# Performance work log

Measured on AMD Instinct MI355X. Metric: run time of the kernel, lower is better.

The kernel has to match this reference:

```python
import jax, jax.numpy as jnp
import numpy as np
from jax import lax

D_MODEL, D_STATE, D_CONV, EXPAND, HEADDIM = 1024, 128, 4, 2, 64
D_INNER = EXPAND * D_MODEL            # 2048
NHEADS = D_INNER // HEADDIM           # 32
CONV_DIM = D_INNER + 2 * D_STATE      # 2304 (ngroups=1)
D_IN_PROJ = 2 * D_INNER + 2 * D_STATE + NHEADS  # 4384


def setup_inputs() -> dict:
    key = jax.random.key(0)
    ks = jax.random.split(key, 9)
    b, l = 2, 2048
    x = jax.random.normal(ks[0], (b, l, D_MODEL), jnp.float32)
    in_proj_w = jax.random.normal(ks[1], (D_IN_PROJ, D_MODEL), jnp.float32) * 0.02
    conv_w = jax.random.normal(ks[2], (CONV_DIM, D_CONV), jnp.float32) * 0.2
    conv_b = jax.random.normal(ks[3], (CONV_DIM,), jnp.float32) * 0.02
    dt_bias = jnp.log(jnp.expm1(jax.random.uniform(ks[4], (NHEADS,), jnp.float32, 0.001, 0.1)))
    A_log = jnp.log(jax.random.uniform(ks[5], (NHEADS,), jnp.float32, 1.0, 16.0))
    D = jax.random.normal(ks[6], (NHEADS,), jnp.float32)
    norm_w = jnp.ones((D_INNER,), jnp.float32)
    out_proj_w = jax.random.normal(ks[7], (D_MODEL, D_INNER), jnp.float32) * 0.02
    return {"x": x, "in_proj_w": in_proj_w, "conv_w": conv_w, "conv_b": conv_b,
            "dt_bias": dt_bias, "A_log": A_log, "D": D, "norm_w": norm_w,
            "out_proj_w": out_proj_w}


def _mamba2(x, in_proj_w, conv_w, conv_b, dt_bias, A_log, D, norm_w, out_proj_w):
    b, l, _ = x.shape
    zxbcdt = x @ in_proj_w.T  # (b,l,D_IN_PROJ)
    z = zxbcdt[..., :D_INNER]
    xBC = zxbcdt[..., D_INNER:D_INNER + CONV_DIM]
    dt = zxbcdt[..., D_INNER + CONV_DIM:]  # (b,l,h)
    # causal depthwise conv1d + SiLU
    xBC_pad = jnp.pad(xBC, ((0, 0), (D_CONV - 1, 0), (0, 0)))
    windows = jnp.stack([xBC_pad[:, k:k + l, :] for k in range(D_CONV)], axis=-1)  # (b,l,c,K)
    xBC = jax.nn.silu(jnp.einsum('blck,ck->blc', windows, conv_w) + conv_b)
    xs = xBC[..., :D_INNER]
    B = xBC[..., D_INNER:D_INNER + D_STATE]   # (b,l,n)
    C = xBC[..., D_INNER + D_STATE:]          # (b,l,n)
    xh = xs.reshape(b, l, NHEADS, HEADDIM)
    dt = jax.nn.softplus(dt + dt_bias)        # (b,l,h)
    A = -jnp.exp(A_log)                       # (h,)
    dA = jnp.exp(dt * A)                      # (b,l,h)
    xdt = xh * dt[..., None]                  # (b,l,h,p)

    def step(S, inp):
        dA_t, xdt_t, B_t, C_t = inp  # (b,h),(b,h,p),(b,n),(b,n)
        S = dA_t[:, :, None, None] * S + xdt_t[..., None] * B_t[:, None, None, :]
        y_t = jnp.einsum('bhpn,bn->bhp', S, C_t)
        return S, y_t

    S0 = jnp.zeros((b, NHEADS, HEADDIM, D_STATE), x.dtype)
    _, y = lax.scan(step, S0,
                    (dA.transpose(1, 0, 2), xdt.transpose(1, 0, 2, 3),
                     B.transpose(1, 0, 2), C.transpose(1, 0, 2)))
    y = y.transpose(1, 0, 2, 3) + D[None, None, :, None] * xh  # (b,l,h,p)
    y = y.reshape(b, l, D_INNER)
    # gated RMSNorm: norm(y * silu(z)) * weight
    y = y * jax.nn.silu(z)
    y = y * lax.rsqrt(jnp.mean(y * y, axis=-1, keepdims=True) + 1e-5) * norm_w
    return y @ out_proj_w.T


def reference(x, in_proj_w, conv_w, conv_b, dt_bias, A_log, D, norm_w, out_proj_w):
    return x + _mamba2(x, in_proj_w, conv_w, conv_b, dt_bias, A_log, D, norm_w, out_proj_w)
```

## Files before the change

### kernel.cpp

```cpp
#include <hip/hip_runtime.h>
#include <hip/hip_bf16.h>
#include <cstdint>

typedef __hip_bfloat16 bf16;
typedef __attribute__((ext_vector_type(8))) short short8;
typedef __attribute__((ext_vector_type(4))) float f32x4;
typedef unsigned int u32;

#define BB 2
#define LL 2048
#define DM 1024
#define DI 2048
#define DS 128
#define NH 32
#define HD 64
#define CONVD 2304
#define DPROJ 4384
#define DPAD 4480
#define NBL (BB*LL)
#define NCHK 16
#define CLEN 128

__device__ __forceinline__ float bf2f(bf16 v) { return __bfloat162float(v); }
__device__ __forceinline__ bf16 f2bf(float f) { return __float2bfloat16(f); }
__device__ __forceinline__ unsigned short f2bfu(float f) {
  bf16 t = __float2bfloat16(f); return *(unsigned short*)&t;
}
__device__ __forceinline__ float bfu2f(unsigned short u) {
  u32 b = ((u32)u) << 16; return *(float*)&b;
}

__device__ __forceinline__ void gload16(const void* g, void* l) {
  __builtin_amdgcn_global_load_lds(
      (const __attribute__((address_space(1))) u32*)g,
      (__attribute__((address_space(3))) u32*)l, 16, 0, 0);
}

template<int N> __device__ __forceinline__ void waitvm() {
  __builtin_amdgcn_sched_barrier(0);
  if constexpr (N == 0) asm volatile("s_waitcnt vmcnt(0)" ::: "memory");
  else if constexpr (N == 3) asm volatile("s_waitcnt vmcnt(3)" ::: "memory");
  else if constexpr (N == 4) asm volatile("s_waitcnt vmcnt(4)" ::: "memory");
  __builtin_amdgcn_sched_barrier(0);
}
__device__ __forceinline__ void rawbar() {
  __builtin_amdgcn_sched_barrier(0);
  __builtin_amdgcn_s_barrier();
  __builtin_amdgcn_sched_barrier(0);
}

__global__ __launch_bounds__(256)
void k_cast3(const float* __restrict__ s0, bf16* __restrict__ d0, int n0,
             const float* __restrict__ s1, bf16* __restrict__ d1, int n1,
             const float* __restrict__ s2, bf16* __restrict__ d2, int n2)
{
  int i = blockIdx.x * blockDim.x + threadIdx.x;
  const int stride = gridDim.x * blockDim.x;
  const int total = n0 + n1 + n2;
  for (; i < total; i += stride) {
    const float* s; bf16* d; int j = i;
    if (j < n0)            { s = s0; d = d0; }
    else if (j < n0 + n1)  { s = s1; d = d1; j -= n0; }
    else                   { s = s2; d = d2; j -= n0 + n1; }
    const float4 v = ((const float4*)s)[j];
    u32 w0 = (u32)f2bfu(v.x) | ((u32)f2bfu(v.y) << 16);
    u32 w1 = (u32)f2bfu(v.z) | ((u32)f2bfu(v.w) << 16);
    *(uint2*)(d + (size_t)j*4) = make_uint2(w0, w1);
  }
}

template<int TM, int MODE>
__global__ __launch_bounds__(512)
void k_gemm_nt(const bf16* __restrict__ A, const bf16* __restrict__ W,
               int K, int Nw, int ldo,
               float* __restrict__ outf, const bf16* __restrict__ residb,
               bf16* __restrict__ outb, float* __restrict__ dtraw)
{
  constexpr int BUFE = (TM + 128) * 64;
  constexpr int LPT  = TM/64 + 2;
  __shared__ __align__(16) unsigned short S[2*BUFE];
  const int tid = threadIdx.x;
  const int w = tid >> 6, lane = tid & 63;
  const int m0 = blockIdx.x * TM, n0 = blockIdx.y * 128;
  const int wr = w >> 2, wc = w & 3;
  constexpr int MI = TM / 32;
  f32x4 acc[MI][2] = {};
  const int r0 = lane & 15;
  const int kq = (lane >> 4) * 8;
  const int srow = lane >> 3;
  const int scol = ((lane & 7) ^ (lane >> 3)) << 3;
  const int swz  = (r0 & 7) << 3;
  const int NT = K >> 6;

#define STAGE(T, BUF) {                                                          \
    const int k0s = (T) << 6;                                                    \
    unsigned short* dst = S + (BUF) * BUFE;                                      \
    _Pragma("unroll")                                                            \
    for (int it = 0; it < TM/64; ++it) {                                         \
      const int seg = it*8 + w;                                                  \
      const int row = seg*8 + srow;                                              \
      gload16(A + (size_t)(m0 + row)*K + (k0s + scol), (char*)dst + seg*1024);   \
    }                                                                            \
    unsigned short* dstW = dst + TM*64;                                          \
    _Pragma("unroll")                                                            \
    for (int it = 0; it < 2; ++it) {                                             \
      const int seg = it*8 + w;                                                  \
      const int row = seg*8 + srow;                                              \
      int rw = n0 + row; rw = (rw < Nw) ? rw : (Nw - 1);                         \
      gload16(W + (size_t)rw*K + (k0s + scol), (char*)dstW + seg*1024);          \
    }                                                                            \
  }

  STAGE(0, 0);
  STAGE(1, 1);
  waitvm<LPT>();
  rawbar();

  for (int t = 0; t < NT; ++t) {
    const int cur = t & 1;
    const unsigned short* As = S + cur*BUFE;
    const unsigned short* Ws = As + TM*64;
    #pragma unroll
    for (int kk = 0; kk < 64; kk += 32) {
      const int ce = (kk + kq) ^ swz;
      short8 af[MI], bw[2];
      #pragma unroll
      for (int mi = 0; mi < MI; ++mi)
        af[mi] = *(const short8*)(As + (wr*(TM/2) + mi*16 + r0)*64 + ce);
      #pragma unroll
      for (int ni = 0; ni < 2; ++ni)
        bw[ni] = *(const short8*)(Ws + (wc*32 + ni*16 + r0)*64 + ce);
      #pragma unroll
      for (int mi = 0; mi < MI; ++mi)
        #pragma unroll
        for (int ni = 0; ni < 2; ++ni)
          acc[mi][ni] = __builtin_amdgcn_mfma_f32_16x16x32_bf16(af[mi], bw[ni], acc[mi][ni], 0, 0, 0);
    }
    rawbar();
    if (t + 2 < NT) {
      STAGE(t + 2, cur);
      waitvm<LPT>();
      rawbar();
    } else if (t + 1 < NT) {
      waitvm<0>();
      rawbar();
    }
  }
#undef STAGE

  const int rr = (lane >> 4) * 4;
  if (MODE == 0) {
    #pragma unroll
    for (int mi = 0; mi < MI; ++mi) {
      #pragma unroll
      for (int ni = 0; ni < 2; ++ni) {
        const int col = n0 + wc*32 + ni*16 + r0;
        #pragma unroll
        for (int r = 0; r < 4; ++r) {
          const int row = m0 + wr*(TM/2) + mi*16 + rr + r;
          outf[(size_t)row*ldo + col] =
              acc[mi][ni][r] + bf2f(residb[(size_t)row*ldo + col]);
        }
      }
    }
  } else {
    if (n0 == 4352 && wc == 0) {
      #pragma unroll
      for (int ni = 0; ni < 2; ++ni)
        #pragma unroll
        for (int mi = 0; mi < MI; ++mi)
          #pragma unroll
          for (int r = 0; r < 4; ++r) {
            const int row = m0 + wr*(TM/2) + mi*16 + rr + r;
            dtraw[(size_t)row*NH + ni*16 + r0] = acc[mi][ni][r];
          }
    }
    #pragma unroll
    for (int mi = 0; mi < MI; ++mi) {
      #pragma unroll
      for (int ni = 0; ni < 2; ++ni) {
        const int colt = wc*32 + ni*16 + r0;
        #pragma unroll
        for (int r = 0; r < 4; ++r) {
          const int rowt = wr*(TM/2) + mi*16 + rr + r;
          const int g = (colt >> 3) ^ (rowt & 7);
          S[rowt*128 + g*8 + (colt & 7)] = f2bfu(acc[mi][ni][r]);
        }
      }
    }
    __syncthreads();
    const int row = tid >> 2, j4 = tid & 3;
    unsigned short* orow = (unsigned short*)outb + (size_t)(m0 + row)*ldo + n0 + j4*32;
    #pragma unroll
    for (int jj = 0; jj < 4; ++jj) {
      const int g = (j4*4 + jj) ^ (row & 7);
      *(short8*)(orow + jj*8) = *(const short8*)&S[row*128 + g*8];
    }
  }
}

__global__ __launch_bounds__(256)
void k_conv(const bf16* __restrict__ zxb, const float* __restrict__ dtraw,
            const float* __restrict__ convw, const float* __restrict__ convb,
            const float* __restrict__ dtb, const float* __restrict__ alog,
            bf16* __restrict__ xs, float* __restrict__ dt,
            float* __restrict__ ldA, bf16* __restrict__ Bc, bf16* __restrict__ Cc)
{
  const int bl = ((blockIdx.x & 7) << 9) | (blockIdx.x >> 3);
  const int l = bl & (LL - 1);
  const int tid = threadIdx.x;
  if (tid < NH) {
    float raw = dtraw[(size_t)bl*NH + tid] + dtb[tid];
    float sp = (raw > 20.f) ? raw : log1pf(__expf(raw));
    float Ah = -__expf(alog[tid]);
    dt[(size_t)bl*NH + tid] = sp;
    ldA[(size_t)bl*NH + tid] = sp * Ah;
  }
  for (int g = tid; g < CONVD/8; g += 256) {
    const int c0 = g*8;
    float acc[8];
    float4 wv[8];
    #pragma unroll
    for (int e = 0; e < 8; ++e) wv[e] = ((const float4*)convw)[c0 + e];
    {
      const float4 b0 = *(const float4*)(convb + c0);
      const float4 b1 = *(const float4*)(convb + c0 + 4);
      acc[0]=b0.x; acc[1]=b0.y; acc[2]=b0.z; acc[3]=b0.w;
      acc[4]=b1.x; acc[5]=b1.y; acc[6]=b1.z; acc[7]=b1.w;
    }
    #pragma unroll
    for (int k = 0; k < 4; ++k) {
      if (l - 3 + k >= 0) {
        short8 v = *(const short8*)((const unsigned short*)zxb + (size_t)(bl - 3 + k)*DPAD + DI + c0);
        #pragma unroll
        for (int e = 0; e < 8; ++e) {
          const float wk = (k == 0) ? wv[e].x : (k == 1) ? wv[e].y : (k == 2) ? wv[e].z : wv[e].w;
          acc[e] = fmaf(bfu2f((unsigned short)v[e]), wk, acc[e]);
        }
      }
    }
    short8 ov;
    #pragma unroll
    for (int e = 0; e < 8; ++e) {
      const float s = acc[e] / (1.f + __expf(-acc[e]));
      ov[e] = (short)f2bfu(s);
    }
    if (c0 < DI)            *(short8*)((unsigned short*)xs + (size_t)bl*DI + c0) = ov;
    else if (c0 < DI + DS)  *(short8*)((unsigned short*)Bc + (size_t)bl*DS + (c0 - DI)) = ov;
    else                    *(short8*)((unsigned short*)Cc + (size_t)bl*DS + (c0 - DI - DS)) = ov;
  }
}

__global__ __launch_bounds__(256)
void k_bt(const bf16* __restrict__ Bc, bf16* __restrict__ BT)
{
  const int bidx2 = blockIdx.x;
  const int b = bidx2 >> 4, c = bidx2 & 15;
  const int bl0 = b*LL + c*CLEN;
  __shared__ unsigned short LT[128*132];
  const int tid = threadIdx.x;
  {
    const int ts = tid >> 3, seg = tid & 7;
    #pragma unroll
    for (int r = 0; r < 4; ++r) {
      const int t = r*32 + ts;
      const unsigned short* src = (const unsigned short*)(Bc + (size_t)(bl0 + t)*DS);
      short8 v0 = *(const short8*)(src + seg*16);
      short8 v1 = *(const short8*)(src + seg*16 + 8);
      u32 w0 = (u32)(unsigned short)v0[0] | ((u32)(unsigned short)v0[1] << 16);
      u32 w1 = (u32)(unsigned short)v0[2] | ((u32)(unsigned short)v0[3] << 16);
      u32 w2 = (u32)(unsigned short)v0[4] | ((u32)(unsigned short)v0[5] << 16);
      u32 w3 = (u32)(unsigned short)v0[6] | ((u32)(unsigned short)v0[7] << 16);
      u32 w4 = (u32)(unsigned short)v1[0] | ((u32)(unsigned short)v1[1] << 16);
      u32 w5 = (u32)(unsigned short)v1[2] | ((u32)(unsigned short)v1[3] << 16);
      u32 w6 = (u32)(unsigned short)v1[4] | ((u32)(unsigned short)v1[5] << 16);
      u32 w7 = (u32)(unsigned short)v1[6] | ((u32)(unsigned short)v1[7] << 16);
      uint2* d = (uint2*)&LT[t*132 + seg*16];
      d[0] = make_uint2(w0, w1); d[1] = make_uint2(w2, w3);
      d[2] = make_uint2(w4, w5); d[3] = make_uint2(w6, w7);
    }
  }
  __syncthreads();
  {
    const int n = tid >> 1, th = tid & 1;
    unsigned short* dst = (unsigned short*)(BT + (size_t)bidx2*16384 + n*128 + th*64);
    #pragma unroll
    for (int j = 0; j < 8; ++j) {
      short8 o;
      #pragma unroll
      for (int e = 0; e < 8; ++e)
        o[e] = (short)LT[(th*64 + j*8 + e)*132 + n];
      *(short8*)(dst + j*8) = o;
    }
  }
}

__global__ __launch_bounds__(512)
void k_xt_state(const bf16* __restrict__ xs, const float* __restrict__ dt,
                const bf16* __restrict__ BT, const float* __restrict__ ldA,
                bf16* __restrict__ xT, unsigned short* __restrict__ Sloc,
                float* __restrict__ clog)
{
  const int bidx = blockIdx.x;
  const int c = bidx & 15, h = (bidx >> 4) & 31, b = bidx >> 9;
  const int bl0 = b*LL + c*CLEN;
  const int bidx2 = b*NCHK + c;
  __shared__ unsigned short LT[128*68];
  __shared__ __align__(16) unsigned short XWs[64*136];
  __shared__ float w1[128];
  const int tid = threadIdx.x;
  const int w = tid >> 6, lane = tid & 63;
  const int r0 = lane & 15, kq = (lane >> 4) * 8;
  short8 bfr[4];
  #pragma unroll
  for (int kk = 0; kk < 4; ++kk)
    bfr[kk] = *(const short8*)((const unsigned short*)BT + (size_t)bidx2*16384
                               + (size_t)(w*16 + r0)*128 + kk*32 + kq);
  {
    const int ts = tid >> 3, seg = tid & 7;
    #pragma unroll
    for (int r = 0; r < 2; ++r) {
      const int t = r*64 + ts;
      const float dtv = dt[(size_t)(bl0 + t)*NH + h];
      short8 v = *(const short8*)((const unsigned short*)(xs + (size_t)(bl0 + t)*DI + h*HD) + seg*8);
      unsigned short o[8];
      #pragma unroll
      for (int e = 0; e < 8; ++e)
        o[e] = f2bfu(bfu2f((unsigned short)v[e]) * dtv);
      uint2* d = (uint2*)&LT[t*68 + seg*8];
      d[0] = make_uint2((u32)o[0] | ((u32)o[1] << 16), (u32)o[2] | ((u32)o[3] << 16));
      d[1] = make_uint2((u32)o[4] | ((u32)o[5] << 16), (u32)o[6] | ((u32)o[7] << 16));
    }
  }
  if (tid < 64) {
    const int ln = tid;
    const float a0 = ldA[(size_t)(bl0 + 2*ln)*NH + h];
    const float a1 = ldA[(size_t)(bl0 + 2*ln + 1)*NH + h];
    float s = a0 + a1;
    #pragma unroll
    for (int off = 1; off < 64; off <<= 1) {
      const float v = __shfl_up(s, off);
      if (ln >= off) s += v;
    }
    const float Ltot = __shfl(s, 63);
    w1[2*ln + 1] = __expf(Ltot - s);
    w1[2*ln]     = __expf(Ltot - (s - a1));
    if (ln == 63) clog[bidx] = Ltot;
  }
  __syncthreads();
  {
    const int p = tid >> 3, tg = tid & 7;
    unsigned short* xdst = (unsigned short*)xT + (size_t)bidx*8192 + p*128 + tg*16;
    #pragma unroll
    for (int half = 0; half < 2; ++half) {
      short8 oXT, oXW;
      #pragma unroll
      for (int e = 0; e < 8; ++e) {
        const int t = tg*16 + half*8 + e;
        const unsigned short u = LT[t*68 + p];
        oXT[e] = (short)u;
        oXW[e] = (short)f2bfu(bfu2f(u) * w1[t]);
      }
      *(short8*)(xdst + half*8) = oXT;
      *(short8*)&XWs[p*136 + tg*16 + half*8] = oXW;
    }
  }
  __syncthreads();
  f32x4 acc[4] = {};
  #pragma unroll
  for (int kk = 0; kk < 4; ++kk) {
    #pragma unroll
    for (int mi = 0; mi < 4; ++mi) {
      short8 a = *(const short8*)&XWs[(mi*16 + r0)*136 + kk*32 + kq];
      acc[mi] = __builtin_amdgcn_mfma_f32_16x16x32_bf16(a, bfr[kk], acc[mi], 0, 0, 0);
    }
  }
  const int rr = (lane >> 4) * 4;
  unsigned short* So = Sloc + (size_t)bidx*8192;
  #pragma unroll
  for (int mi = 0; mi < 4; ++mi)
    #pragma unroll
    for (int r = 0; r < 4; ++r)
      So[(mi*16 + rr + r)*128 + w*16 + r0] = f2bfu(acc[mi][r]);
}

__global__ __launch_bounds__(256)
void k_chunk_combine(unsigned short* __restrict__ Sloc, const float* __restrict__ clog)
{
  const int bh = blockIdx.x >> 3;
  const int e0 = ((blockIdx.x & 7) * 256 + threadIdx.x) * 4;
  float t0 = 0.f, t1 = 0.f, t2 = 0.f, t3 = 0.f;
  for (int c = 0; c < NCHK; ++c) {
    unsigned short* Sp = Sloc + ((size_t)(bh*NCHK + c))*8192 + e0;
    const uint2 raw = *(const uint2*)Sp;
    const float l0 = bfu2f((unsigned short)(raw.x & 0xffff));
    const float l1 = bfu2f((unsigned short)(raw.x >> 16));
    const float l2 = bfu2f((unsigned short)(raw.y & 0xffff));
    const float l3 = bfu2f((unsigned short)(raw.y >> 16));
    uint2 o;
    o.x = (u32)f2bfu(t0) | ((u32)f2bfu(t1) << 16);
    o.y = (u32)f2bfu(t2) | ((u32)f2bfu(t3) << 16);
    *(uint2*)Sp = o;
    const float P = __expf(clog[bh*NCHK + c]);
    t0 = P*t0 + l0; t1 = P*t1 + l1; t2 = P*t2 + l2; t3 = P*t3 + l3;
  }
}

__global__ __launch_bounds__(512)
void k_scan(const bf16* __restrict__ xT, const bf16* __restrict__ Bc,
            const bf16* __restrict__ Cc, const unsigned short* __restrict__ Sinit,
            const float* __restrict__ ldA, const bf16* __restrict__ xs,
            const float* __restrict__ Dv, unsigned short* __restrict__ y)
{
  const int bidx = blockIdx.x;
  const int c = bidx & 15, h = (bidx >> 4) & 31, b = bidx >> 9;
  const int bl0 = b*LL + c*CLEN;
  __shared__ __align__(16) unsigned short Bs[128*136];
  __shared__ __align__(16) unsigned short XDs[64*136];
  __shared__ __align__(16) unsigned short SIs[64*136];
  __shared__ float la[128];
  const int tid = threadIdx.x;
  const int w = tid >> 6, lane = tid & 63;
  const int r0 = lane & 15, kq = (lane >> 4) * 8;
  short8 cfr[4];
  #pragma unroll
  for (int kk = 0; kk < 4; ++kk)
    cfr[kk] = *(const short8*)((const unsigned short*)Cc
                               + (size_t)(bl0 + w*16 + r0)*DS + kk*32 + kq);
  {
    const int t = tid >> 2, sg = tid & 3;
    const unsigned short* sb = (const unsigned short*)(Bc + (size_t)(bl0 + t)*DS) + sg*32;
    #pragma unroll
    for (int j = 0; j < 4; ++j)
      *(short8*)&Bs[t*136 + sg*32 + j*8] = *(const short8*)(sb + j*8);
  }
  {
    const int p = tid >> 3, seg = tid & 7;
    const unsigned short* sx = (const unsigned short*)(xT + (size_t)bidx*8192 + p*128) + seg*16;
    *(short8*)&XDs[p*136 + seg*16]     = *(const short8*)sx;
    *(short8*)&XDs[p*136 + seg*16 + 8] = *(const short8*)(sx + 8);
    const unsigned short* sp = Sinit + (size_t)bidx*8192 + p*128 + seg*16;
    *(short8*)&SIs[p*136 + seg*16]     = *(const short8*)sp;
    *(short8*)&SIs[p*136 + seg*16 + 8] = *(const short8*)(sp + 8);
  }
  if (tid < 64) {
    const int ln = tid;
    const float a0 = ldA[(size_t)(bl0 + 2*ln)*NH + h];
    const float a1 = ldA[(size_t)(bl0 + 2*ln + 1)*NH + h];
    float s = a0 + a1;
    #pragma unroll
    for (int off = 1; off < 64; off <<= 1) {
      const float v = __shfl_up(s, off);
      if (ln >= off) s += v;
    }
    la[2*ln + 1] = s;
    la[2*ln]     = s - a1;
  }
  __syncthreads();

  const int trow = w*16 + (lane >> 4) * 4;

  f32x4 aG[8] = {};
  f32x4 aU[4] = {};
  #pragma unroll
  for (int kk = 0; kk < 4; ++kk) {
    #pragma unroll
    for (int sf = 0; sf < 8; ++sf) {
      short8 bb = *(const short8*)&Bs[(sf*16 + r0)*136 + kk*32 + kq];
      aG[sf] = __builtin_amdgcn_mfma_f32_16x16x32_bf16(cfr[kk], bb, aG[sf], 0, 0, 0);
    }
    #pragma unroll
    for (int pf = 0; pf < 4; ++pf) {
      short8 bs = *(const short8*)&SIs[(pf*16 + r0)*136 + kk*32 + kq];
      aU[pf] = __builtin_amdgcn_mfma_f32_16x16x32_bf16(cfr[kk], bs, aU[pf], 0, 0, 0);
    }
  }
  __syncthreads();
  float lat[4];
  #pragma unroll
  for (int r = 0; r < 4; ++r) lat[r] = la[trow + r];
  #pragma unroll
  for (int sf = 0; sf < 8; ++sf) {
    const int s = sf*16 + r0;
    const float las = la[s];
    #pragma unroll
    for (int r = 0; r < 4; ++r) {
      const int t = trow + r;
      const float m = (s <= t) ? aG[sf][r] * __expf(lat[r] - las) : 0.f;
      Bs[t*136 + s] = f2bfu(m);
    }
  }
  __syncthreads();
  f32x4 aY[4] = {};
  #pragma unroll
  for (int kk = 0; kk < 4; ++kk) {
    short8 a = *(const short8*)&Bs[(w*16 + r0)*136 + kk*32 + kq];
    #pragma unroll
    for (int pf = 0; pf < 4; ++pf) {
      short8 bx = *(const short8*)&XDs[(pf*16 + r0)*136 + kk*32 + kq];
      aY[pf] = __builtin_amdgcn_mfma_f32_16x16x32_bf16(a, bx, aY[pf], 0, 0, 0);
    }
  }
  const float Dh = Dv[h];
  float el[4];
  #pragma unroll
  for (int r = 0; r < 4; ++r) el[r] = __expf(lat[r]);
  #pragma unroll
  for (int pf = 0; pf < 4; ++pf) {
    #pragma unroll
    for (int r = 0; r < 4; ++r) {
      const int t = trow + r, p = pf*16 + r0;
      const size_t gi = (size_t)(bl0 + t)*DI + h*HD + p;
      const float yv = aY[pf][r] + el[r]*aU[pf][r] + Dh*bfu2f(((const unsigned short*)xs)[gi]);
      y[gi] = f2bfu(yv);
    }
  }
}

__global__ __launch_bounds__(256)
void k_gate_norm(const unsigned short* __restrict__ y, const bf16* __restrict__ zxb,
                 const float* __restrict__ nw, bf16* __restrict__ yn)
{
  const size_t bl = blockIdx.x;
  const int tid = threadIdx.x;
  const int c0 = tid * 8;
  short8 yv8 = *(const short8*)(y + bl*DI + c0);
  short8 zv = *(const short8*)((const unsigned short*)zxb + bl*DPAD + c0);
  float v[8];
  float acc = 0.f;
  #pragma unroll
  for (int e = 0; e < 8; ++e) {
    const float zf = bfu2f((unsigned short)zv[e]);
    v[e] = bfu2f((unsigned short)yv8[e]) * (zf / (1.f + __expf(-zf)));
    acc += v[e]*v[e];
  }
  #pragma unroll
  for (int off = 32; off > 0; off >>= 1) acc += __shfl_down(acc, off);
  __shared__ float red[4];
  if ((tid & 63) == 0) red[tid >> 6] = acc;
  __syncthreads();
  const float total = red[0] + red[1] + red[2] + red[3];
  const float r = rsqrtf(total * (1.f/DI) + 1e-5f);
  const float4 w0 = *(const float4*)(nw + c0);
  const float4 w1 = *(const float4*)(nw + c0 + 4);
  const float wv[8] = {w0.x, w0.y, w0.z, w0.w, w1.x, w1.y, w1.z, w1.w};
  short8 ov;
  #pragma unroll
  for (int e = 0; e < 8; ++e) ov[e] = (short)f2bfu(v[e] * r * wv[e]);
  *(short8*)((unsigned short*)yn + bl*DI + c0) = ov;
}

extern "C" void kernel_launch(void* const* d_in, const int* in_sizes, int n_in,
                              void* d_out, int out_size, void* d_ws, size_t ws_size,
                              hipStream_t stream)
{
  const float* x     = (const float*)d_in[0];
  const float* inw   = (const float*)d_in[1];
  const float* convw = (const float*)d_in[2];
  const float* convb = (const float*)d_in[3];
  const float* dtb   = (const float*)d_in[4];
  const float* alog  = (const float*)d_in[5];
  const float* Dv    = (const float*)d_in[6];
  const float* nw    = (const float*)d_in[7];
  const float* outw  = (const float*)d_in[8];
  float* out = (float*)d_out;
  char* ws = (char*)d_ws;

  constexpr size_t OFF_ZX   = 0;
  constexpr size_t OFF_DTRAW= OFF_ZX   + (size_t)NBL*DPAD*2;
  constexpr size_t OFF_XS   = OFF_DTRAW+ (size_t)NBL*NH*4;
  constexpr size_t OFF_DT   = OFF_XS   + (size_t)NBL*DI*2;
  constexpr size_t OFF_LDA  = OFF_DT   + (size_t)NBL*NH*4;
  constexpr size_t OFF_B    = OFF_LDA  + (size_t)NBL*NH*4;
  constexpr size_t OFF_C    = OFF_B    + (size_t)NBL*DS*2;
  constexpr size_t OFF_XT   = OFF_C    + (size_t)NBL*DS*2;
  constexpr size_t OFF_BT   = OFF_XT   + (size_t)1024*8192*2;
  constexpr size_t OFF_SLOC = OFF_BT   + (size_t)32*16384*2;
  constexpr size_t OFF_CLOG = OFF_SLOC + (size_t)1024*8192*2;
  constexpr size_t OFF_Y    = OFF_CLOG + 4096;
  constexpr size_t OFF_YN   = OFF_Y    + (size_t)NBL*DI*2;
  constexpr size_t OFF_XB   = OFF_YN   + (size_t)NBL*DI*2;
  constexpr size_t OFF_INWB = OFF_XB   + (size_t)NBL*DM*2;
  constexpr size_t OFF_OUTWB= OFF_INWB + (size_t)DPROJ*DM*2;

  bf16*  zxb  = (bf16*) (ws + OFF_ZX);
  float* dtraw= (float*)(ws + OFF_DTRAW);
  bf16*  xs   = (bf16*) (ws + OFF_XS);
  float* dt   = (float*)(ws + OFF_DT);
  float* ldA  = (float*)(ws + OFF_LDA);
  bf16*  Bcp  = (bf16*) (ws + OFF_B);
  bf16*  Ccp  = (bf16*) (ws + OFF_C);
  bf16*  xT   = (bf16*) (ws + OFF_XT);
  bf16*  BT   = (bf16*) (ws + OFF_BT);
  unsigned short* Sloc = (unsigned short*)(ws + OFF_SLOC);
  float* clog = (float*)(ws + OFF_CLOG);
  unsigned short* yb = (unsigned short*)(ws + OFF_Y);
  bf16*  yn   = (bf16*) (ws + OFF_YN);
  bf16*  xb   = (bf16*) (ws + OFF_XB);
  bf16*  inwb = (bf16*) (ws + OFF_INWB);
  bf16*  outwb= (bf16*) (ws + OFF_OUTWB);

  k_cast3<<<2048, 256, 0, stream>>>(x, xb, NBL*DM/4,
                                    inw, inwb, DPROJ*DM/4,
                                    outw, outwb, DM*DI/4);
  k_gemm_nt<128,1><<<dim3(32, 35), 512, 0, stream>>>(xb, inwb, DM, DPROJ, DPAD, nullptr, nullptr, zxb, dtraw);
  k_conv<<<NBL, 256, 0, stream>>>(zxb, dtraw, convw, convb, dtb, alog, xs, dt, ldA, Bcp, Ccp);
  k_bt<<<BB*NCHK, 256, 0, stream>>>(Bcp, BT);
  k_xt_state<<<BB*NH*NCHK, 512, 0, stream>>>(xs, dt, BT, ldA, xT, Sloc, clog);
  k_chunk_combine<<<64*8, 256, 0, stream>>>(Sloc, clog);
  k_scan<<<BB*NH*NCHK, 512, 0, stream>>>(xT, Bcp, Ccp, Sloc, ldA, xs, Dv, yb);
  k_gate_norm<<<NBL, 256, 0, stream>>>(yb, zxb, nw, yn);
  k_gemm_nt<64,0><<<dim3(64, 8), 512, 0, stream>>>(yn, outwb, DI, DM, DM, out, xb, nullptr, nullptr);
}
```

Before: 194.8 us.

## Drop B and x transpose buffers; transpose in LDS inside state and scan kernels

Removes the separate k_bt launch and the global xT intermediate. k_xt_state now loads B rows into shared memory and builds its MFMA fragments through a strided LDS transpose. k_scan reloads xs and dt directly and forms x*dt transposed in LDS. This saves one kernel launch and roughly 16 MB of global write+read traffic, at the cost of extra LDS usage, an extra barrier, and redundant B loads across heads.

```diff
diff --git a/kernel.cpp b/kernel.cpp
--- a/kernel.cpp
+++ b/kernel.cpp
@@ -251,71 +251,21 @@
   }
 }
 
-__global__ __launch_bounds__(256)
-void k_bt(const bf16* __restrict__ Bc, bf16* __restrict__ BT)
-{
-  const int bidx2 = blockIdx.x;
-  const int b = bidx2 >> 4, c = bidx2 & 15;
-  const int bl0 = b*LL + c*CLEN;
-  __shared__ unsigned short LT[128*132];
-  const int tid = threadIdx.x;
-  {
-    const int ts = tid >> 3, seg = tid & 7;
-    #pragma unroll
-    for (int r = 0; r < 4; ++r) {
-      const int t = r*32 + ts;
-      const unsigned short* src = (const unsigned short*)(Bc + (size_t)(bl0 + t)*DS);
-      short8 v0 = *(const short8*)(src + seg*16);
-      short8 v1 = *(const short8*)(src + seg*16 + 8);
-      u32 w0 = (u32)(unsigned short)v0[0] | ((u32)(unsigned short)v0[1] << 16);
-      u32 w1 = (u32)(unsigned short)v0[2] | ((u32)(unsigned short)v0[3] << 16);
-      u32 w2 = (u32)(unsigned short)v0[4] | ((u32)(unsigned short)v0[5] << 16);
-      u32 w3 = (u32)(unsigned short)v0[6] | ((u32)(unsigned short)v0[7] << 16);
-      u32 w4 = (u32)(unsigned short)v1[0] | ((u32)(unsigned short)v1[1] << 16);
-      u32 w5 = (u32)(unsigned short)v1[2] | ((u32)(unsigned short)v1[3] << 16);
-      u32 w6 = (u32)(unsigned short)v1[4] | ((u32)(unsigned short)v1[5] << 16);
-      u32 w7 = (u32)(unsigned short)v1[6] | ((u32)(unsigned short)v1[7] << 16);
-      uint2* d = (uint2*)&LT[t*132 + seg*16];
-      d[0] = make_uint2(w0, w1); d[1] = make_uint2(w2, w3);
-      d[2] = make_uint2(w4, w5); d[3] = make_uint2(w6, w7);
-    }
-  }
-  __syncthreads();
-  {
-    const int n = tid >> 1, th = tid & 1;
-    unsigned short* dst = (unsigned short*)(BT + (size_t)bidx2*16384 + n*128 + th*64);
-    #pragma unroll
-    for (int j = 0; j < 8; ++j) {
-      short8 o;
-      #pragma unroll
-      for (int e = 0; e < 8; ++e)
-        o[e] = (short)LT[(th*64 + j*8 + e)*132 + n];
-      *(short8*)(dst + j*8) = o;
-    }
-  }
-}
-
 __global__ __launch_bounds__(512)
 void k_xt_state(const bf16* __restrict__ xs, const float* __restrict__ dt,
-                const bf16* __restrict__ BT, const float* __restrict__ ldA,
-                bf16* __restrict__ xT, unsigned short* __restrict__ Sloc,
-                float* __restrict__ clog)
+                const bf16* __restrict__ Bc, const float* __restrict__ ldA,
+                unsigned short* __restrict__ Sloc, float* __restrict__ clog)
 {
   const int bidx = blockIdx.x;
   const int c = bidx & 15, h = (bidx >> 4) & 31, b = bidx >> 9;
   const int bl0 = b*LL + c*CLEN;
-  const int bidx2 = b*NCHK + c;
   __shared__ unsigned short LT[128*68];
+  __shared__ unsigned short BL[128*132];
   __shared__ __align__(16) unsigned short XWs[64*136];
   __shared__ float w1[128];
   const int tid = threadIdx.x;
   const int w = tid >> 6, lane = tid & 63;
   const int r0 = lane & 15, kq = (lane >> 4) * 8;
-  short8 bfr[4];
-  #pragma unroll
-  for (int kk = 0; kk < 4; ++kk)
-    bfr[kk] = *(const short8*)((const unsigned short*)BT + (size_t)bidx2*16384
-                               + (size_t)(w*16 + r0)*128 + kk*32 + kq);
   {
     const int ts = tid >> 3, seg = tid & 7;
     #pragma unroll
@@ -332,6 +282,13 @@
       d[1] = make_uint2((u32)o[4] | ((u32)o[5] << 16), (u32)o[6] | ((u32)o[7] << 16));
     }
   }
+  {
+    const int t = tid >> 2, q = tid & 3;
+    const unsigned short* sb = (const unsigned short*)Bc + (size_t)(bl0 + t)*DS + q*32;
+    #pragma unroll
+    for (int j = 0; j < 4; ++j)
+      *(short8*)&BL[t*132 + q*32 + j*8] = *(const short8*)(sb + j*8);
+  }
   if (tid < 64) {
     const int ln = tid;
     const float a0 = ldA[(size_t)(bl0 + 2*ln)*NH + h];
@@ -348,20 +305,28 @@
     if (ln == 63) clog[bidx] = Ltot;
   }
   __syncthreads();
+  short8 bfr[4];
+  {
+    const int n = w*16 + r0;
+    #pragma unroll
+    for (int kk = 0; kk < 4; ++kk) {
+      short8 o;
+      #pragma unroll
+      for (int e = 0; e < 8; ++e)
+        o[e] = (short)BL[(kk*32 + kq + e)*132 + n];
+      bfr[kk] = o;
+    }
+  }
   {
     const int p = tid >> 3, tg = tid & 7;
-    unsigned short* xdst = (unsigned short*)xT + (size_t)bidx*8192 + p*128 + tg*16;
     #pragma unroll
     for (int half = 0; half < 2; ++half) {
-      short8 oXT, oXW;
+      short8 oXW;
       #pragma unroll
       for (int e = 0; e < 8; ++e) {
         const int t = tg*16 + half*8 + e;
-        const unsigned short u = LT[t*68 + p];
-        oXT[e] = (short)u;
-        oXW[e] = (short)f2bfu(bfu2f(u) * w1[t]);
+        oXW[e] = (short)f2bfu(bfu2f(LT[t*68 + p]) * w1[t]);
       }
-      *(short8*)(xdst + half*8) = oXT;
       *(short8*)&XWs[p*136 + tg*16 + half*8] = oXW;
     }
   }
@@ -407,9 +372,9 @@
 }
 
 __global__ __launch_bounds__(512)
-void k_scan(const bf16* __restrict__ xT, const bf16* __restrict__ Bc,
-            const bf16* __restrict__ Cc, const unsigned short* __restrict__ Sinit,
-            const float* __restrict__ ldA, const bf16* __restrict__ xs,
+void k_scan(const bf16* __restrict__ xs, const float* __restrict__ dt,
+            const bf16* __restrict__ Bc, const bf16* __restrict__ Cc,
+            const unsigned short* __restrict__ Sinit, const float* __restrict__ ldA,
             const float* __restrict__ Dv, unsigned short* __restrict__ y)
 {
   const int bidx = blockIdx.x;
@@ -419,6 +384,7 @@
   __shared__ __align__(16) unsigned short XDs[64*136];
   __shared__ __align__(16) unsigned short SIs[64*136];
   __shared__ float la[128];
+  __shared__ float dts[128];
   const int tid = threadIdx.x;
   const int w = tid >> 6, lane = tid & 63;
   const int r0 = lane & 15, kq = (lane >> 4) * 8;
@@ -435,10 +401,14 @@
       *(short8*)&Bs[t*136 + sg*32 + j*8] = *(const short8*)(sb + j*8);
   }
   {
+    const int t = tid >> 2, q = tid & 3;
+    const unsigned short* sx = (const unsigned short*)xs + (size_t)(bl0 + t)*DI + h*HD + q*16;
+    *(short8*)&XDs[t*68 + q*16]     = *(const short8*)sx;
+    *(short8*)&XDs[t*68 + q*16 + 8] = *(const short8*)(sx + 8);
+  }
+  if (tid < 128) dts[tid] = dt[(size_t)(bl0 + tid)*NH + h];
+  {
     const int p = tid >> 3, seg = tid & 7;
-    const unsigned short* sx = (const unsigned short*)(xT + (size_t)bidx*8192 + p*128) + seg*16;
-    *(short8*)&XDs[p*136 + seg*16]     = *(const short8*)sx;
-    *(short8*)&XDs[p*136 + seg*16 + 8] = *(const short8*)(sx + 8);
     const unsigned short* sp = Sinit + (size_t)bidx*8192 + p*128 + seg*16;
     *(short8*)&SIs[p*136 + seg*16]     = *(const short8*)sp;
     *(short8*)&SIs[p*136 + seg*16 + 8] = *(const short8*)(sp + 8);
@@ -455,6 +425,22 @@
     }
     la[2*ln + 1] = s;
     la[2*ln]     = s - a1;
+  }
+  __syncthreads();
+  float xdv[16];
+  {
+    const int px = tid >> 3, tg = tid & 7;
+    #pragma unroll
+    for (int e = 0; e < 16; ++e) {
+      const int t = tg*16 + e;
+      xdv[e] = bfu2f(XDs[t*68 + px]) * dts[t];
+    }
+    __syncthreads();
+    short8 o0, o1;
+    #pragma unroll
+    for (int e = 0; e < 8; ++e) { o0[e] = (short)f2bfu(xdv[e]); o1[e] = (short)f2bfu(xdv[8+e]); }
+    *(short8*)&XDs[px*136 + tg*16]     = o0;
+    *(short8*)&XDs[px*136 + tg*16 + 8] = o1;
   }
   __syncthreads();
 
@@ -573,9 +559,7 @@
   constexpr size_t OFF_LDA  = OFF_DT   + (size_t)NBL*NH*4;
   constexpr size_t OFF_B    = OFF_LDA  + (size_t)NBL*NH*4;
   constexpr size_t OFF_C    = OFF_B    + (size_t)NBL*DS*2;
-  constexpr size_t OFF_XT   = OFF_C    + (size_t)NBL*DS*2;
-  constexpr size_t OFF_BT   = OFF_XT   + (size_t)1024*8192*2;
-  constexpr size_t OFF_SLOC = OFF_BT   + (size_t)32*16384*2;
+  constexpr size_t OFF_SLOC = OFF_C    + (size_t)NBL*DS*2;
   constexpr size_t OFF_CLOG = OFF_SLOC + (size_t)1024*8192*2;
   constexpr size_t OFF_Y    = OFF_CLOG + 4096;
   constexpr size_t OFF_YN   = OFF_Y    + (size_t)NBL*DI*2;
@@ -590,8 +574,6 @@
   float* ldA  = (float*)(ws + OFF_LDA);
   bf16*  Bcp  = (bf16*) (ws + OFF_B);
   bf16*  Ccp  = (bf16*) (ws + OFF_C);
-  bf16*  xT   = (bf16*) (ws + OFF_XT);
-  bf16*  BT   = (bf16*) (ws + OFF_BT);
   unsigned short* Sloc = (unsigned short*)(ws + OFF_SLOC);
   float* clog = (float*)(ws + OFF_CLOG);
   unsigned short* yb = (unsigned short*)(ws + OFF_Y);
@@ -605,10 +587,9 @@
                                     outw, outwb, DM*DI/4);
   k_gemm_nt<128,1><<<dim3(32, 35), 512, 0, stream>>>(xb, inwb, DM, DPROJ, DPAD, nullptr, nullptr, zxb, dtraw);
   k_conv<<<NBL, 256, 0, stream>>>(zxb, dtraw, convw, convb, dtb, alog, xs, dt, ldA, Bcp, Ccp);
-  k_bt<<<BB*NCHK, 256, 0, stream>>>(Bcp, BT);
-  k_xt_state<<<BB*NH*NCHK, 512, 0, stream>>>(xs, dt, BT, ldA, xT, Sloc, clog);
+  k_xt_state<<<BB*NH*NCHK, 512, 0, stream>>>(xs, dt, Bcp, ldA, Sloc, clog);
   k_chunk_combine<<<64*8, 256, 0, stream>>>(Sloc, clog);
-  k_scan<<<BB*NH*NCHK, 512, 0, stream>>>(xT, Bcp, Ccp, Sloc, ldA, xs, Dv, yb);
+  k_scan<<<BB*NH*NCHK, 512, 0, stream>>>(xs, dt, Bcp, Ccp, Sloc, ldA, Dv, yb);
   k_gate_norm<<<NBL, 256, 0, stream>>>(yb, zxb, nw, yn);
   k_gemm_nt<64,0><<<dim3(64, 8), 512, 0, stream>>>(yn, outwb, DI, DM, DM, out, xb, nullptr, nullptr);
 }
```

After: 205.5 us. 1.05x slower.

## Triple-buffer MODE 0 GEMM pipeline and raise wave priority around MFMA blocks

Applied to the files above, without the earlier changes.

For the MODE 0 GEMM (out_proj with residual), the shared-memory pipeline moves from two buffers to three. The prefetch of tile t+2 is issued before computing tile t, so each iteration needs only one barrier instead of two. s_setprio(1)/s_setprio(0) brackets are also placed around the MFMA loops in the GEMM and in the chunk-state and chunk-output kernels, so the scheduler favours waves that are issuing matrix ops. The extra buffer raises LDS use for MODE 0, which may lower occupancy.

```diff
diff --git a/kernel.cpp b/kernel.cpp
--- a/kernel.cpp
+++ b/kernel.cpp
@@ -78,7 +78,8 @@
 {
   constexpr int BUFE = (TM + 128) * 64;
   constexpr int LPT  = TM/64 + 2;
-  __shared__ __align__(16) unsigned short S[2*BUFE];
+  constexpr int NBUF = (MODE == 0) ? 3 : 2;
+  __shared__ __align__(16) unsigned short S[NBUF*BUFE];
   const int tid = threadIdx.x;
   const int w = tid >> 6, lane = tid & 63;
   const int m0 = blockIdx.x * TM, n0 = blockIdx.y * 128;
@@ -116,34 +117,66 @@
   waitvm<LPT>();
   rawbar();
 
-  for (int t = 0; t < NT; ++t) {
-    const int cur = t & 1;
-    const unsigned short* As = S + cur*BUFE;
-    const unsigned short* Ws = As + TM*64;
-    #pragma unroll
-    for (int kk = 0; kk < 64; kk += 32) {
-      const int ce = (kk + kq) ^ swz;
-      short8 af[MI], bw[2];
-      #pragma unroll
-      for (int mi = 0; mi < MI; ++mi)
-        af[mi] = *(const short8*)(As + (wr*(TM/2) + mi*16 + r0)*64 + ce);
-      #pragma unroll
-      for (int ni = 0; ni < 2; ++ni)
-        bw[ni] = *(const short8*)(Ws + (wc*32 + ni*16 + r0)*64 + ce);
-      #pragma unroll
-      for (int mi = 0; mi < MI; ++mi)
+  if (MODE == 0) {
+    for (int t = 0; t < NT; ++t) {
+      const int cur = t % 3;
+      if (t + 2 < NT) STAGE(t + 2, (t + 2) % 3);
+      const unsigned short* As = S + cur*BUFE;
+      const unsigned short* Ws = As + TM*64;
+      __builtin_amdgcn_s_setprio(1);
+      #pragma unroll
+      for (int kk = 0; kk < 64; kk += 32) {
+        const int ce = (kk + kq) ^ swz;
+        short8 af[MI], bw[2];
+        #pragma unroll
+        for (int mi = 0; mi < MI; ++mi)
+          af[mi] = *(const short8*)(As + (wr*(TM/2) + mi*16 + r0)*64 + ce);
         #pragma unroll
         for (int ni = 0; ni < 2; ++ni)
-          acc[mi][ni] = __builtin_amdgcn_mfma_f32_16x16x32_bf16(af[mi], bw[ni], acc[mi][ni], 0, 0, 0);
-    }
-    rawbar();
-    if (t + 2 < NT) {
-      STAGE(t + 2, cur);
-      waitvm<LPT>();
+          bw[ni] = *(const short8*)(Ws + (wc*32 + ni*16 + r0)*64 + ce);
+        #pragma unroll
+        for (int mi = 0; mi < MI; ++mi)
+          #pragma unroll
+          for (int ni = 0; ni < 2; ++ni)
+            acc[mi][ni] = __builtin_amdgcn_mfma_f32_16x16x32_bf16(af[mi], bw[ni], acc[mi][ni], 0, 0, 0);
+      }
+      __builtin_amdgcn_s_setprio(0);
+      if (t + 1 < NT) {
+        if (t + 2 < NT) waitvm<LPT>();
+        else            waitvm<0>();
+        rawbar();
+      }
+    }
+  } else {
+    for (int t = 0; t < NT; ++t) {
+      const int cur = t & 1;
+      const unsigned short* As = S + cur*BUFE;
+      const unsigned short* Ws = As + TM*64;
+      #pragma unroll
+      for (int kk = 0; kk < 64; kk += 32) {
+        const int ce = (kk + kq) ^ swz;
+        short8 af[MI], bw[2];
+        #pragma unroll
+        for (int mi = 0; mi < MI; ++mi)
+          af[mi] = *(const short8*)(As + (wr*(TM/2) + mi*16 + r0)*64 + ce);
+        #pragma unroll
+        for (int ni = 0; ni < 2; ++ni)
+          bw[ni] = *(const short8*)(Ws + (wc*32 + ni*16 + r0)*64 + ce);
+        #pragma unroll
+        for (int mi = 0; mi < MI; ++mi)
+          #pragma unroll
+          for (int ni = 0; ni < 2; ++ni)
+            acc[mi][ni] = __builtin_amdgcn_mfma_f32_16x16x32_bf16(af[mi], bw[ni], acc[mi][ni], 0, 0, 0);
+      }
       rawbar();
-    } else if (t + 1 < NT) {
-      waitvm<0>();
-      rawbar();
+      if (t + 2 < NT) {
+        STAGE(t + 2, cur);
+        waitvm<LPT>();
+        rawbar();
+      } else if (t + 1 < NT) {
+        waitvm<0>();
+        rawbar();
+      }
     }
   }
 #undef STAGE
@@ -367,6 +400,7 @@
   }
   __syncthreads();
   f32x4 acc[4] = {};
+  __builtin_amdgcn_s_setprio(1);
   #pragma unroll
   for (int kk = 0; kk < 4; ++kk) {
     #pragma unroll
@@ -375,6 +409,7 @@
       acc[mi] = __builtin_amdgcn_mfma_f32_16x16x32_bf16(a, bfr[kk], acc[mi], 0, 0, 0);
     }
   }
+  __builtin_amdgcn_s_setprio(0);
   const int rr = (lane >> 4) * 4;
   unsigned short* So = Sloc + (size_t)bidx*8192;
   #pragma unroll
@@ -462,6 +497,7 @@
 
   f32x4 aG[8] = {};
   f32x4 aU[4] = {};
+  __builtin_amdgcn_s_setprio(1);
   #pragma unroll
   for (int kk = 0; kk < 4; ++kk) {
     #pragma unroll
@@ -475,6 +511,7 @@
       aU[pf] = __builtin_amdgcn_mfma_f32_16x16x32_bf16(cfr[kk], bs, aU[pf], 0, 0, 0);
     }
   }
+  __builtin_amdgcn_s_setprio(0);
   __syncthreads();
   float lat[4];
   #pragma unroll
@@ -492,6 +529,7 @@
   }
   __syncthreads();
   f32x4 aY[4] = {};
+  __builtin_amdgcn_s_setprio(1);
   #pragma unroll
   for (int kk = 0; kk < 4; ++kk) {
     short8 a = *(const short8*)&Bs[(w*16 + r0)*136 + kk*32 + kq];
@@ -501,6 +539,7 @@
       aY[pf] = __builtin_amdgcn_mfma_f32_16x16x32_bf16(a, bx, aY[pf], 0, 0, 0);
     }
   }
+  __builtin_amdgcn_s_setprio(0);
   const float Dh = Dv[h];
   float el[4];
   #pragma unroll
```

Measured after the change: 195.7 us. No clear change (+0.5%).
